# Optimization experiments

Hardware: AMD Instinct MI355X
Metric: run time of the kernel (lower is better)

The kernel has to match this reference:

```python
import jax, jax.numpy as jnp
import numpy as np

D = 3  # hardcoded window half-width in the module


def setup_inputs() -> dict:
    key = jax.random.key(0)
    ks = jax.random.split(key, 5)
    B, T, S = 16, 1024, 4096
    q_size, c_size, p_size = 512, 512, 512
    q = jax.random.normal(ks[0], (B, q_size, S), jnp.float32)
    c_t = jax.random.normal(ks[1], (B, T, c_size), jnp.float32)
    # torch nn.Linear weight layouts: (out_features, in_features)
    W_a = jax.random.normal(ks[2], (c_size, q_size), jnp.float32) / np.sqrt(q_size).astype(np.float32)
    W_p = jax.random.normal(ks[3], (p_size, c_size), jnp.float32) / np.sqrt(c_size).astype(np.float32)
    V_p = jax.random.normal(ks[4], (1, p_size), jnp.float32) / np.sqrt(p_size).astype(np.float32)
    return {"q": q, "c_t": c_t, "W_a": W_a, "W_p": W_p, "V_p": V_p}


def reference(q, c_t, W_a, W_p, V_p):
    B, q_size, S = q.shape
    # predictive alignment: p_t = S * sigmoid(V_p tanh(W_p c_t)) -> (B, T, 1)
    p_t = S * jax.nn.sigmoid(jnp.tanh(c_t @ W_p.T) @ V_p.T)
    # pad one NaN column at the front of the sequence, then (B, S+1, q_size)
    q_pad = jnp.pad(q, ((0, 0), (0, 0), (1, 0)), constant_values=jnp.nan).transpose(0, 2, 1)
    # window indices: clamp(long(p_t) + idx + 1, 0, S+1) % (S+1), idx in [-D, D]
    offsets = jnp.arange(-D + 1, D + 2)  # (2D+1,)
    s = jnp.clip(p_t.astype(jnp.int32) + offsets[None, None, :], 0, S + 1) % (S + 1)  # (B,T,2D+1)
    # per-batch gather of the local window: (B, T, 2D+1, q_size)
    qg = q_pad[jnp.arange(B)[:, None, None], s]
    nan_loc = jnp.isnan(qg[..., 0])  # (B, T, 2D+1)
    qg = jnp.where(nan_loc[..., None], 0.0, qg)
    # score: dot(W_a q, c_t) -> (B, T, 2D+1)
    a_t = jnp.einsum('btwq,cq,btc->btw', qg, W_a, c_t)
    a_t = jnp.where(nan_loc, -jnp.inf, a_t)
    attn = jax.nn.softmax(a_t, axis=2)
    # Gaussian decay around predicted position p_t
    gauss = jnp.exp(-2.0 * ((jnp.clip(s.astype(jnp.float32) - 1.0, 0.0, None) - p_t) / D) ** 2)
    W_attn = attn * gauss
    out = jnp.einsum('btw,btwq->btq', W_attn, qg)  # (B, T, q_size)
    return out
```

## Files before the change

### kernel.cpp

```cpp
#include <hip/hip_runtime.h>
#include <hip/hip_bf16.h>

#define BB 16
#define TT 1024
#define SS 4096
#define CS 512
#define QS 512
#define PS 512
#define NROW (BB*TT)

typedef unsigned short ushort_t;
typedef unsigned int u32;
typedef short bf16x8 __attribute__((ext_vector_type(8)));
typedef float f32x4 __attribute__((ext_vector_type(4)));

#define AS1 __attribute__((address_space(1)))
#define AS3 __attribute__((address_space(3)))

__device__ __forceinline__ void gl2l16(const void* g, void* l) {
    __builtin_amdgcn_global_load_lds((const AS1 u32*)g, (AS3 u32*)l, 16, 0, 0);
}

__device__ __forceinline__ ushort_t f2bf(float f) {
    u32 x = __float_as_uint(f);
    return (ushort_t)((x + 0x7fffu + ((x >> 16) & 1u)) >> 16);
}
__device__ __forceinline__ float bf2f(ushort_t b) {
    return __uint_as_float(((u32)b) << 16);
}

__global__ __launch_bounds__(256) void k_conv_a(const float* __restrict__ c,
                                                ushort_t* __restrict__ A) {
    const int i = blockIdx.x * 256 + threadIdx.x;
    const int m = i >> 7;
    const int k = (i & 127) * 4;
    float4 v = *(const float4*)(c + (size_t)m * CS + k);
    ushort4 hi, lo;
    hi.x = f2bf(v.x); lo.x = f2bf(v.x - bf2f(hi.x));
    hi.y = f2bf(v.y); lo.y = f2bf(v.y - bf2f(hi.y));
    hi.z = f2bf(v.z); lo.z = f2bf(v.z - bf2f(hi.z));
    hi.w = f2bf(v.w); lo.w = f2bf(v.w - bf2f(hi.w));
    *(ushort4*)(A + (size_t)m * 1024 + k)       = hi;
    *(ushort4*)(A + (size_t)m * 1024 + 512 + k) = lo;
}

__global__ __launch_bounds__(256) void k_conv_b(const float* __restrict__ Wa,
                                                const float* __restrict__ Wp,
                                                ushort_t* __restrict__ B,
                                                int* __restrict__ cnt) {
    const int n = blockIdx.x;
    const int t = threadIdx.x;
    if (n == 0 && t < 2) cnt[t] = 0;
    #pragma unroll
    for (int kk = 0; kk < 2; ++kk) {
        const int k = t + 256 * kk;
        float v = (n < 512) ? Wa[(size_t)k * QS + n] : Wp[(size_t)(n - 512) * CS + k];
        ushort_t hi = f2bf(v);
        ushort_t lo = f2bf(v - bf2f(hi));
        B[(size_t)n * 1024 + k]       = hi;
        B[(size_t)n * 1024 + 512 + k] = lo;
    }
}

__global__ __launch_bounds__(256) void k_tq(const float* __restrict__ q,
                                            float* __restrict__ qT) {
    const int b  = blockIdx.z;
    const int s0 = blockIdx.x * 64 + (threadIdx.x & 15) * 4;
    const int d0 = blockIdx.y * 64 + (threadIdx.x >> 4) * 4;
    const float* qb = q + ((size_t)b * QS + d0) * SS + s0;
    float4 v0 = *(const float4*)(qb);
    float4 v1 = *(const float4*)(qb + SS);
    float4 v2 = *(const float4*)(qb + 2 * SS);
    float4 v3 = *(const float4*)(qb + 3 * SS);
    float* qo = qT + ((size_t)b * SS + s0) * QS + d0;
    *(float4*)(qo)          = make_float4(v0.x, v1.x, v2.x, v3.x);
    *(float4*)(qo + QS)     = make_float4(v0.y, v1.y, v2.y, v3.y);
    *(float4*)(qo + 2 * QS) = make_float4(v0.z, v1.z, v2.z, v3.z);
    *(float4*)(qo + 3 * QS) = make_float4(v0.w, v1.w, v2.w, v3.w);
}

__global__ __launch_bounds__(1024, 4) void k_gemm(const ushort_t* __restrict__ A,
                                                  const ushort_t* __restrict__ B,
                                                  const float* __restrict__ V_p,
                                                  float* __restrict__ u,
                                                  float* __restrict__ zpart) {
    __shared__ ushort_t lds[8][8192];
    const int tid = threadIdx.x;
    const int l = tid & 63;
    const int w = tid >> 6;
    const int wm = w >> 2;
    const int wn = w & 3;
    const int ln = l & 15, lh = l >> 4;

    const int orig = blockIdx.x;
    const int swz = ((orig & 7) << 5) + (orig >> 3);
    const int m0 = (swz >> 2) * 256;
    const int nt = swz & 3;
    const int n0 = nt * 256;

    const int srow = tid >> 2;
    const int scg  = tid & 3;
    const int scol0 = (scg ^ ((srow >> 1) & 3)) * 8;

    const int swzr = (lh ^ ((ln >> 1) & 3)) << 3;
    int aoffL[4], boffL[4];
    #pragma unroll
    for (int mi = 0; mi < 4; ++mi)
        aoffL[mi] = (wm * 64 + mi * 16 + ln) * 32 + swzr;
    #pragma unroll
    for (int ni = 0; ni < 4; ++ni)
        boffL[ni] = (wn * 64 + ni * 16 + ln) * 32 + swzr;

    f32x4 acc[4][4];
    #pragma unroll
    for (int a = 0; a < 4; ++a)
        #pragma unroll
        for (int b2 = 0; b2 < 4; ++b2) acc[a][b2] = (f32x4){0.f, 0.f, 0.f, 0.f};

    auto STAGE = [&](int c) {
        const int tt = c >> 2, rem = c & 3, kh = rem >> 1;
        const int blk = tt >> 3, k0 = (tt & 7) << 6;
        const ushort_t* src;
        if (rem & 1) {
            const int boff = (blk == 1) ? 512 : 0;
            src = B + (size_t)(n0 + srow) * 1024 + boff + k0 + kh * 32 + scol0;
        } else {
            const int aoff = (blk == 2) ? 512 : 0;
            src = A + (size_t)(m0 + srow) * 1024 + aoff + k0 + kh * 32 + scol0;
        }
        gl2l16(src, &lds[c & 7][tid * 8]);
    };

    #pragma unroll
    for (int c = 0; c < 4; ++c) STAGE(c);
    asm volatile("s_waitcnt vmcnt(0)" ::: "memory");
    __builtin_amdgcn_s_barrier();

    #pragma unroll 1
    for (int t = 0; t < 24; ++t) {
        if (t < 23) {
            #pragma unroll
            for (int i = 0; i < 4; ++i) STAGE(4 * t + 4 + i);
        }
        {
            const ushort_t* bA = &lds[(4 * t) & 7][0];
            const ushort_t* bB = &lds[(4 * t + 1) & 7][0];
            bf16x8 af[4], bb[4];
            #pragma unroll
            for (int mi = 0; mi < 4; ++mi)
                af[mi] = *(const bf16x8*)(bA + aoffL[mi]);
            #pragma unroll
            for (int ni = 0; ni < 4; ++ni)
                bb[ni] = *(const bf16x8*)(bB + boffL[ni]);
            __builtin_amdgcn_s_setprio(1);
            #pragma unroll
            for (int mi = 0; mi < 4; ++mi)
                #pragma unroll
                for (int ni = 0; ni < 4; ++ni)
                    acc[mi][ni] = __builtin_amdgcn_mfma_f32_16x16x32_bf16(
                        af[mi], bb[ni], acc[mi][ni], 0, 0, 0);
            __builtin_amdgcn_s_setprio(0);
        }
        {
            const ushort_t* bA = &lds[(4 * t + 2) & 7][0];
            const ushort_t* bB = &lds[(4 * t + 3) & 7][0];
            bf16x8 af[4], bb[4];
            #pragma unroll
            for (int mi = 0; mi < 4; ++mi)
                af[mi] = *(const bf16x8*)(bA + aoffL[mi]);
            #pragma unroll
            for (int ni = 0; ni < 4; ++ni)
                bb[ni] = *(const bf16x8*)(bB + boffL[ni]);
            __builtin_amdgcn_s_setprio(1);
            #pragma unroll
            for (int mi = 0; mi < 4; ++mi)
                #pragma unroll
                for (int ni = 0; ni < 4; ++ni)
                    acc[mi][ni] = __builtin_amdgcn_mfma_f32_16x16x32_bf16(
                        af[mi], bb[ni], acc[mi][ni], 0, 0, 0);
            __builtin_amdgcn_s_setprio(0);
        }
        asm volatile("s_waitcnt vmcnt(0)" ::: "memory");
        __builtin_amdgcn_s_barrier();
    }

    if (nt < 2) {
        #pragma unroll
        for (int mi = 0; mi < 4; ++mi) {
            #pragma unroll
            for (int r = 0; r < 4; ++r) {
                const int m = m0 + wm * 64 + mi * 16 + lh * 4 + r;
                float* up = u + (size_t)m * QS + nt * 256 + wn * 64 + ln;
                #pragma unroll
                for (int ni = 0; ni < 4; ++ni) up[ni * 16] = acc[mi][ni][r];
            }
        }
    } else {
        float vp[4];
        #pragma unroll
        for (int ni = 0; ni < 4; ++ni)
            vp[ni] = V_p[(nt - 2) * 256 + wn * 64 + ni * 16 + ln];
        #pragma unroll
        for (int mi = 0; mi < 4; ++mi) {
            #pragma unroll
            for (int r = 0; r < 4; ++r) {
                float sv = 0.f;
                #pragma unroll
                for (int ni = 0; ni < 4; ++ni) sv += tanhf(acc[mi][ni][r]) * vp[ni];
                sv += __shfl_xor(sv, 1, 64);
                sv += __shfl_xor(sv, 2, 64);
                sv += __shfl_xor(sv, 4, 64);
                sv += __shfl_xor(sv, 8, 64);
                if (ln == 0)
                    zpart[(size_t)(m0 + wm * 64 + mi * 16 + lh * 4 + r) * 8 +
                          (nt - 2) * 4 + wn] = sv;
            }
        }
    }
}

__global__ __launch_bounds__(256) void k_z(const float* __restrict__ zpart,
                                           float* __restrict__ pt, int* __restrict__ tr,
                                           int* __restrict__ list1, int* __restrict__ cnt1) {
    const int row = blockIdx.x * 256 + threadIdx.x;
    const float4 a = *(const float4*)(zpart + (size_t)row * 8);
    const float4 b = *(const float4*)(zpart + (size_t)row * 8 + 4);
    float z = ((a.x + a.y) + (a.z + a.w)) + ((b.x + b.y) + (b.z + b.w));
    float ptv = 4096.f / (1.f + expf(-z));
    float fr = ptv - floorf(ptv);
    pt[row] = ptv;
    tr[row] = (int)ptv;
    if (fr < 0.06f || fr > 0.94f) {
        int i = atomicAdd(cnt1, 1);
        list1[i] = row;
    }
}

__global__ __launch_bounds__(256) void k_rep1(
    const float* __restrict__ c_t, const float* __restrict__ W_p,
    const float* __restrict__ V_p, float* __restrict__ pt, int* __restrict__ tr,
    const int* __restrict__ list1, const int* __restrict__ cnt1,
    int* __restrict__ list2, int* __restrict__ cnt2)
{
    const int tid = threadIdx.x;
    const int lane = tid & 63;
    const int wid = tid >> 6;
    const int n1 = cnt1[0];
    __shared__ float cl[8][132 * 4];
    __shared__ double zl[4][8];
    __shared__ int rows_s[8];

    for (int g0 = blockIdx.x * 8; g0 < n1; g0 += gridDim.x * 8) {
        const int nr = min(8, n1 - g0);
        __syncthreads();
        if (tid < nr) rows_s[tid] = list1[g0 + tid];
        __syncthreads();
        for (int idx = tid; idx < nr * 128; idx += 256) {
            int r = idx >> 7, k = (idx & 127) * 4;
            *(float4*)&cl[r][k] = *(const float4*)(c_t + (size_t)rows_s[r] * CS + k);
        }
        __syncthreads();

        const float* wp0 = W_p + (size_t)tid * CS;
        const float* wp1 = W_p + (size_t)(tid + 256) * CS;
        f32x4 acc[2][8];
        #pragma unroll
        for (int p = 0; p < 2; ++p)
            #pragma unroll
            for (int r = 0; r < 8; ++r) acc[p][r] = (f32x4){0.f, 0.f, 0.f, 0.f};

        for (int k = 0; k < CS; k += 16) {
            f32x4 w0[4], w1[4];
            #pragma unroll
            for (int j = 0; j < 4; ++j) {
                w0[j] = *(const f32x4*)(wp0 + k + 4 * j);
                w1[j] = *(const f32x4*)(wp1 + k + 4 * j);
            }
            #pragma unroll
            for (int j = 0; j < 4; ++j) {
                #pragma unroll
                for (int r = 0; r < 8; ++r) {
                    f32x4 c4 = *(const f32x4*)&cl[r][k + 4 * j];
                    acc[0][r] += c4 * w0[j];
                    acc[1][r] += c4 * w1[j];
                }
            }
        }

        const float vp0 = V_p[tid];
        const float vp1 = V_p[tid + 256];
        double zp[8];
        #pragma unroll
        for (int r = 0; r < 8; ++r) {
            float X0 = (acc[0][r][0] + acc[0][r][1]) + (acc[0][r][2] + acc[0][r][3]);
            float X1 = (acc[1][r][0] + acc[1][r][1]) + (acc[1][r][2] + acc[1][r][3]);
            zp[r] = (double)(tanhf(X0) * vp0) + (double)(tanhf(X1) * vp1);
        }
        #pragma unroll
        for (int r = 0; r < 8; ++r) {
            double v = zp[r];
            #pragma unroll
            for (int o = 32; o > 0; o >>= 1) v += __shfl_down(v, o, 64);
            if (lane == 0) zl[wid][r] = v;
        }
        __syncthreads();
        if (tid < nr) {
            double z = (zl[0][tid] + zl[1][tid]) + (zl[2][tid] + zl[3][tid]);
            double ptv = 4096.0 / (1.0 + exp(-z));
            const int row = rows_s[tid];
            pt[row] = (float)ptv;
            tr[row] = (int)ptv;
            double fr = ptv - floor(ptv);
            if (fr < 5e-3 || fr > 0.995) {
                int i2 = atomicAdd(cnt2, 1);
                list2[i2] = row;
            }
        }
    }
}

__global__ __launch_bounds__(256) void k_rep2a(
    const float* __restrict__ c_t, const float* __restrict__ W_p,
    const float* __restrict__ V_p,
    const int* __restrict__ list2, const int* __restrict__ cnt2,
    double* __restrict__ zp2)
{
    const int tid = threadIdx.x;
    const int pl = tid & 63;
    const int kq = tid >> 6;
    const int n2 = cnt2[0];
    __shared__ float cl[CS];
    __shared__ double xsh[4][64];

    for (int i = blockIdx.x; i < n2 * 8; i += gridDim.x) {
        const int li = i >> 3;
        const int pc = i & 7;
        const int row = list2[li];
        const int p0 = pc * 64;
        __syncthreads();
        if (tid < 128)
            *(float4*)(cl + tid * 4) = *(const float4*)(c_t + (size_t)row * CS + tid * 4);
        __syncthreads();
        const float* wr = W_p + (size_t)(p0 + pl) * CS + kq * 128;
        const float* cr = cl + kq * 128;
        double Xa = 0.0, Xb = 0.0, Xc = 0.0, Xd = 0.0;
        #pragma unroll 4
        for (int k = 0; k < 128; k += 4) {
            float4 w4 = *(const float4*)(wr + k);
            float4 c4 = *(const float4*)(cr + k);
            Xa += (double)c4.x * w4.x;
            Xb += (double)c4.y * w4.y;
            Xc += (double)c4.z * w4.z;
            Xd += (double)c4.w * w4.w;
        }
        xsh[kq][pl] = (Xa + Xb) + (Xc + Xd);
        __syncthreads();
        if (tid < 64) {
            double X = (xsh[0][pl] + xsh[1][pl]) + (xsh[2][pl] + xsh[3][pl]);
            double zv = tanh(X) * (double)V_p[p0 + pl];
            #pragma unroll
            for (int o = 32; o > 0; o >>= 1) zv += __shfl_down(zv, o, 64);
            if (pl == 0) zp2[i] = zv;
        }
    }
}

__global__ __launch_bounds__(256) void k_rep2b(
    const double* __restrict__ zp2, const int* __restrict__ list2,
    const int* __restrict__ cnt2, float* __restrict__ pt, int* __restrict__ tr)
{
    const int idx = blockIdx.x * 256 + threadIdx.x;
    if (idx >= cnt2[0]) return;
    const double* zr = zp2 + (size_t)idx * 8;
    double z = 0.0;
    #pragma unroll
    for (int j = 0; j < 8; ++j) z += zr[j];
    double ptv = 4096.0 / (1.0 + exp(-z));
    const int row = list2[idx];
    pt[row] = (float)ptv;
    tr[row] = (int)ptv;
}

__global__ __launch_bounds__(256) void k_attn_t(
    const float* __restrict__ qT, const float* __restrict__ u,
    const float* __restrict__ pt, const int* __restrict__ tr,
    float* __restrict__ out)
{
    const int wid = threadIdx.x >> 6;
    const int lane = threadIdx.x & 63;
    const int bt = blockIdx.x * 4 + wid;
    const int b = bt >> 10;

    const float* urow = u + (size_t)bt * QS;
    float4 ua = *(const float4*)(urow + lane * 8);
    float4 ub = *(const float4*)(urow + lane * 8 + 4);
    float uv[8] = {ua.x, ua.y, ua.z, ua.w, ub.x, ub.y, ub.z, ub.w};

    const float ptv = pt[bt];
    const int tn = tr[bt];
    const float* qTb = qT + (size_t)b * SS * QS;

    bool val[7];
    int pos[7];
    #pragma unroll
    for (int w = 0; w < 7; ++w) {
        int sv = tn + w - 2;
        sv = sv < 0 ? 0 : (sv > SS + 1 ? SS + 1 : sv);
        if (sv == SS + 1) sv = 0;
        val[w] = (sv != 0);
        pos[w] = sv - 1;
    }

    float qg[7][8];
    #pragma unroll
    for (int w = 0; w < 7; ++w) {
        if (val[w]) {
            const float* qr = qTb + (size_t)pos[w] * QS + lane * 8;
            float4 a = *(const float4*)qr;
            float4 c = *(const float4*)(qr + 4);
            qg[w][0] = a.x; qg[w][1] = a.y; qg[w][2] = a.z; qg[w][3] = a.w;
            qg[w][4] = c.x; qg[w][5] = c.y; qg[w][6] = c.z; qg[w][7] = c.w;
        } else {
            #pragma unroll
            for (int j = 0; j < 8; ++j) qg[w][j] = 0.f;
        }
    }

    float at[7];
    #pragma unroll
    for (int w = 0; w < 7; ++w) {
        float p = 0.f;
        #pragma unroll
        for (int j = 0; j < 8; ++j) p = fmaf(qg[w][j], uv[j], p);
        #pragma unroll
        for (int o = 1; o < 64; o <<= 1) p += __shfl_xor(p, o, 64);
        at[w] = p;
    }

    float m = -1e30f;
    #pragma unroll
    for (int w = 0; w < 7; ++w) if (val[w]) m = fmaxf(m, at[w]);
    float e[7], den = 0.f;
    #pragma unroll
    for (int w = 0; w < 7; ++w) { e[w] = val[w] ? expf(at[w] - m) : 0.f; den += e[w]; }
    const float inv = 1.f / den;

    float acc[8] = {0.f, 0.f, 0.f, 0.f, 0.f, 0.f, 0.f, 0.f};
    #pragma unroll
    for (int w = 0; w < 7; ++w) {
        if (val[w]) {
            float d = ((float)pos[w] - ptv) * (1.f / 3.f);
            float wt = e[w] * inv * expf(-2.f * d * d);
            #pragma unroll
            for (int j = 0; j < 8; ++j) acc[j] = fmaf(wt, qg[w][j], acc[j]);
        }
    }

    float* orow = out + (size_t)bt * QS + lane * 8;
    *(float4*)orow       = make_float4(acc[0], acc[1], acc[2], acc[3]);
    *(float4*)(orow + 4) = make_float4(acc[4], acc[5], acc[6], acc[7]);
}

__global__ __launch_bounds__(256) void k_attn_g(
    const float* __restrict__ q, const float* __restrict__ u,
    const float* __restrict__ pt, const int* __restrict__ tr,
    float* __restrict__ out)
{
    const int wid = threadIdx.x >> 6;
    const int lane = threadIdx.x & 63;
    const int bt = blockIdx.x * 4 + wid;
    const int b = bt >> 10;

    const float* urow = u + (size_t)bt * QS;
    float4 ua = *(const float4*)(urow + lane * 8);
    float4 ub = *(const float4*)(urow + lane * 8 + 4);
    float uv[8] = {ua.x, ua.y, ua.z, ua.w, ub.x, ub.y, ub.z, ub.w};

    const float ptv = pt[bt];
    const int tn = tr[bt];
    const float* qb = q + (size_t)b * QS * SS;

    bool val[7];
    int pos[7];
    #pragma unroll
    for (int w = 0; w < 7; ++w) {
        int sv = tn + w - 2;
        sv = sv < 0 ? 0 : (sv > SS + 1 ? SS + 1 : sv);
        if (sv == SS + 1) sv = 0;
        val[w] = (sv != 0);
        pos[w] = sv - 1;
    }

    float qg[7][8];
    #pragma unroll
    for (int j = 0; j < 8; ++j) {
        const float* qrow = qb + (size_t)(lane * 8 + j) * SS;
        #pragma unroll
        for (int w = 0; w < 7; ++w)
            qg[w][j] = val[w] ? qrow[pos[w]] : 0.f;
    }

    float at[7];
    #pragma unroll
    for (int w = 0; w < 7; ++w) {
        float p = 0.f;
        #pragma unroll
        for (int j = 0; j < 8; ++j) p = fmaf(qg[w][j], uv[j], p);
        #pragma unroll
        for (int o = 1; o < 64; o <<= 1) p += __shfl_xor(p, o, 64);
        at[w] = p;
    }

    float m = -1e30f;
    #pragma unroll
    for (int w = 0; w < 7; ++w) if (val[w]) m = fmaxf(m, at[w]);
    float e[7], den = 0.f;
    #pragma unroll
    for (int w = 0; w < 7; ++w) { e[w] = val[w] ? expf(at[w] - m) : 0.f; den += e[w]; }
    const float inv = 1.f / den;

    float acc[8] = {0.f, 0.f, 0.f, 0.f, 0.f, 0.f, 0.f, 0.f};
    #pragma unroll
    for (int w = 0; w < 7; ++w) {
        if (val[w]) {
            float d = ((float)pos[w] - ptv) * (1.f / 3.f);
            float wt = e[w] * inv * expf(-2.f * d * d);
            #pragma unroll
            for (int j = 0; j < 8; ++j) acc[j] = fmaf(wt, qg[w][j], acc[j]);
        }
    }

    float* orow = out + (size_t)bt * QS + lane * 8;
    *(float4*)orow       = make_float4(acc[0], acc[1], acc[2], acc[3]);
    *(float4*)(orow + 4) = make_float4(acc[4], acc[5], acc[6], acc[7]);
}

extern "C" void kernel_launch(void* const* d_in, const int* in_sizes, int n_in,
                              void* d_out, int out_size, void* d_ws, size_t ws_size,
                              hipStream_t stream) {
    const float* q   = (const float*)d_in[0];
    const float* c_t = (const float*)d_in[1];
    const float* W_a = (const float*)d_in[2];
    const float* W_p = (const float*)d_in[3];
    const float* V_p = (const float*)d_in[4];
    float* out = (float*)d_out;

    char* ws = (char*)d_ws;
    ushort_t* Ap  = (ushort_t*)(ws);
    ushort_t* Bp  = (ushort_t*)(ws + 33554432);
    float*    u   = (float*)  (ws + 35651584);
    float*    zp  = (float*)  (ws + 69206016);
    float*    pt  = (float*)  (ws + 69730304);
    int*      tr  = (int*)    (ws + 69795840);
    int*      l1  = (int*)    (ws + 69861376);
    int*      l2  = (int*)    (ws + 69926912);
    int*      cnt = (int*)    (ws + 69992448);
    double*   zp2 = (double*) (ws + 70000640);
    float*    qT  = (float*)  (ws + 73400320);
    const bool use_T = (ws_size >= 73400320ULL + 134217728ULL);

    hipLaunchKernelGGL(k_conv_a, dim3(8192), dim3(256), 0, stream, c_t, Ap);
    hipLaunchKernelGGL(k_conv_b, dim3(1024), dim3(256), 0, stream, W_a, W_p, Bp, cnt);
    hipLaunchKernelGGL(k_gemm, dim3(256), dim3(1024), 0, stream, Ap, Bp, V_p, u, zp);
    hipLaunchKernelGGL(k_z, dim3(64), dim3(256), 0, stream, zp, pt, tr, l1, cnt);
    hipLaunchKernelGGL(k_rep1, dim3(512), dim3(256), 0, stream,
                       c_t, W_p, V_p, pt, tr, l1, cnt, l2, cnt + 1);
    hipLaunchKernelGGL(k_rep2a, dim3(512), dim3(256), 0, stream,
                       c_t, W_p, V_p, l2, cnt + 1, zp2);
    hipLaunchKernelGGL(k_rep2b, dim3(64), dim3(256), 0, stream,
                       zp2, l2, cnt + 1, pt, tr);
    if (use_T) {
        hipLaunchKernelGGL(k_tq, dim3(64, 8, 16), dim3(256), 0, stream, q, qT);
        hipLaunchKernelGGL(k_attn_t, dim3(NROW / 4), dim3(256), 0, stream, qT, u, pt, tr, out);
    } else {
        hipLaunchKernelGGL(k_attn_g, dim3(NROW / 4), dim3(256), 0, stream, q, u, pt, tr, out);
    }
}
```

Baseline: 238.8 us.

## Fuse q transpose into GEMM main loop and merge conversion kernels

Moves the q transpose (B,QS,S)->(B,S,QS) out of its own kernel and into the GEMM main loop. Each GEMM block loads and stores a slice of q during its first iterations, overlapping that memory traffic with MFMA compute. The two bf16 hi/lo split kernels are also merged into one launch. This saves two kernel launches and hides transpose bandwidth, but adds register pressure and global traffic inside the GEMM loop, which could slow the MFMA pipeline.

```diff
diff --git a/kernel.cpp b/kernel.cpp
--- a/kernel.cpp
+++ b/kernel.cpp
@@ -29,59 +29,46 @@
     return __uint_as_float(((u32)b) << 16);
 }
 
-__global__ __launch_bounds__(256) void k_conv_a(const float* __restrict__ c,
-                                                ushort_t* __restrict__ A) {
-    const int i = blockIdx.x * 256 + threadIdx.x;
-    const int m = i >> 7;
-    const int k = (i & 127) * 4;
-    float4 v = *(const float4*)(c + (size_t)m * CS + k);
-    ushort4 hi, lo;
-    hi.x = f2bf(v.x); lo.x = f2bf(v.x - bf2f(hi.x));
-    hi.y = f2bf(v.y); lo.y = f2bf(v.y - bf2f(hi.y));
-    hi.z = f2bf(v.z); lo.z = f2bf(v.z - bf2f(hi.z));
-    hi.w = f2bf(v.w); lo.w = f2bf(v.w - bf2f(hi.w));
-    *(ushort4*)(A + (size_t)m * 1024 + k)       = hi;
-    *(ushort4*)(A + (size_t)m * 1024 + 512 + k) = lo;
-}
-
-__global__ __launch_bounds__(256) void k_conv_b(const float* __restrict__ Wa,
-                                                const float* __restrict__ Wp,
-                                                ushort_t* __restrict__ B,
-                                                int* __restrict__ cnt) {
-    const int n = blockIdx.x;
+__global__ __launch_bounds__(256) void k_conv(const float* __restrict__ c,
+                                              const float* __restrict__ Wa,
+                                              const float* __restrict__ Wp,
+                                              ushort_t* __restrict__ A,
+                                              ushort_t* __restrict__ B,
+                                              int* __restrict__ cnt) {
+    const int blk = blockIdx.x;
     const int t = threadIdx.x;
-    if (n == 0 && t < 2) cnt[t] = 0;
-    #pragma unroll
-    for (int kk = 0; kk < 2; ++kk) {
-        const int k = t + 256 * kk;
-        float v = (n < 512) ? Wa[(size_t)k * QS + n] : Wp[(size_t)(n - 512) * CS + k];
-        ushort_t hi = f2bf(v);
-        ushort_t lo = f2bf(v - bf2f(hi));
-        B[(size_t)n * 1024 + k]       = hi;
-        B[(size_t)n * 1024 + 512 + k] = lo;
-    }
-}
-
-__global__ __launch_bounds__(256) void k_tq(const float* __restrict__ q,
-                                            float* __restrict__ qT) {
-    const int b  = blockIdx.z;
-    const int s0 = blockIdx.x * 64 + (threadIdx.x & 15) * 4;
-    const int d0 = blockIdx.y * 64 + (threadIdx.x >> 4) * 4;
-    const float* qb = q + ((size_t)b * QS + d0) * SS + s0;
-    float4 v0 = *(const float4*)(qb);
-    float4 v1 = *(const float4*)(qb + SS);
-    float4 v2 = *(const float4*)(qb + 2 * SS);
-    float4 v3 = *(const float4*)(qb + 3 * SS);
-    float* qo = qT + ((size_t)b * SS + s0) * QS + d0;
-    *(float4*)(qo)          = make_float4(v0.x, v1.x, v2.x, v3.x);
-    *(float4*)(qo + QS)     = make_float4(v0.y, v1.y, v2.y, v3.y);
-    *(float4*)(qo + 2 * QS) = make_float4(v0.z, v1.z, v2.z, v3.z);
-    *(float4*)(qo + 3 * QS) = make_float4(v0.w, v1.w, v2.w, v3.w);
+    if (blk < 8192) {
+        const int i = blk * 256 + t;
+        const int m = i >> 7;
+        const int k = (i & 127) * 4;
+        float4 v = *(const float4*)(c + (size_t)m * CS + k);
+        ushort4 hi, lo;
+        hi.x = f2bf(v.x); lo.x = f2bf(v.x - bf2f(hi.x));
+        hi.y = f2bf(v.y); lo.y = f2bf(v.y - bf2f(hi.y));
+        hi.z = f2bf(v.z); lo.z = f2bf(v.z - bf2f(hi.z));
+        hi.w = f2bf(v.w); lo.w = f2bf(v.w - bf2f(hi.w));
+        *(ushort4*)(A + (size_t)m * 1024 + k)       = hi;
+        *(ushort4*)(A + (size_t)m * 1024 + 512 + k) = lo;
+    } else {
+        const int n = blk - 8192;
+        if (n == 0 && t < 2) cnt[t] = 0;
+        #pragma unroll
+        for (int kk = 0; kk < 2; ++kk) {
+            const int k = t + 256 * kk;
+            float v = (n < 512) ? Wa[(size_t)k * QS + n] : Wp[(size_t)(n - 512) * CS + k];
+            ushort_t hi = f2bf(v);
+            ushort_t lo = f2bf(v - bf2f(hi));
+            B[(size_t)n * 1024 + k]       = hi;
+            B[(size_t)n * 1024 + 512 + k] = lo;
+        }
+    }
 }
 
 __global__ __launch_bounds__(1024, 4) void k_gemm(const ushort_t* __restrict__ A,
                                                   const ushort_t* __restrict__ B,
                                                   const float* __restrict__ V_p,
+                                                  const float* __restrict__ q,
+                                                  float* __restrict__ qT,
                                                   float* __restrict__ u,
                                                   float* __restrict__ zpart) {
     __shared__ ushort_t lds[8][8192];
@@ -110,6 +97,12 @@
     #pragma unroll
     for (int ni = 0; ni < 4; ++ni)
         boffL[ni] = (wn * 64 + ni * 16 + ln) * 32 + swzr;
+
+    const int tb = orig >> 4;
+    const int sp = orig & 15;
+    const int sq4 = sp * 256 + (((w & 3) << 4) + ln) * 4;
+    const int dqb = ((w >> 2) << 5) + lh;
+    float4 vq0, vq1, vq2, vq3;
 
     f32x4 acc[4][4];
     #pragma unroll
@@ -138,9 +131,25 @@
 
     #pragma unroll 1
     for (int t = 0; t < 24; ++t) {
+        if (qT && t >= 1 && t <= 8) {
+            const int d0 = (dqb + (t - 1) * 4) * 4;
+            float* dst = qT + ((size_t)tb * SS + sq4) * QS + d0;
+            *(float4*)(dst)          = make_float4(vq0.x, vq1.x, vq2.x, vq3.x);
+            *(float4*)(dst + QS)     = make_float4(vq0.y, vq1.y, vq2.y, vq3.y);
+            *(float4*)(dst + 2 * QS) = make_float4(vq0.z, vq1.z, vq2.z, vq3.z);
+            *(float4*)(dst + 3 * QS) = make_float4(vq0.w, vq1.w, vq2.w, vq3.w);
+        }
         if (t < 23) {
             #pragma unroll
             for (int i = 0; i < 4; ++i) STAGE(4 * t + 4 + i);
+        }
+        if (qT && t < 8) {
+            const int d0 = (dqb + t * 4) * 4;
+            const float* src = q + ((size_t)tb * QS + d0) * SS + sq4;
+            vq0 = *(const float4*)(src);
+            vq1 = *(const float4*)(src + SS);
+            vq2 = *(const float4*)(src + 2 * SS);
+            vq3 = *(const float4*)(src + 3 * SS);
         }
         {
             const ushort_t* bA = &lds[(4 * t) & 7][0];
@@ -559,9 +568,10 @@
     float*    qT  = (float*)  (ws + 73400320);
     const bool use_T = (ws_size >= 73400320ULL + 134217728ULL);
 
-    hipLaunchKernelGGL(k_conv_a, dim3(8192), dim3(256), 0, stream, c_t, Ap);
-    hipLaunchKernelGGL(k_conv_b, dim3(1024), dim3(256), 0, stream, W_a, W_p, Bp, cnt);
-    hipLaunchKernelGGL(k_gemm, dim3(256), dim3(1024), 0, stream, Ap, Bp, V_p, u, zp);
+    hipLaunchKernelGGL(k_conv, dim3(9216), dim3(256), 0, stream,
+                       c_t, W_a, W_p, Ap, Bp, cnt);
+    hipLaunchKernelGGL(k_gemm, dim3(256), dim3(1024), 0, stream,
+                       Ap, Bp, V_p, q, use_T ? qT : (float*)nullptr, u, zp);
     hipLaunchKernelGGL(k_z, dim3(64), dim3(256), 0, stream, zp, pt, tr, l1, cnt);
     hipLaunchKernelGGL(k_rep1, dim3(512), dim3(256), 0, stream,
                        c_t, W_p, V_p, pt, tr, l1, cnt, l2, cnt + 1);
@@ -569,10 +579,8 @@
                        c_t, W_p, V_p, l2, cnt + 1, zp2);
     hipLaunchKernelGGL(k_rep2b, dim3(64), dim3(256), 0, stream,
                        zp2, l2, cnt + 1, pt, tr);
-    if (use_T) {
-        hipLaunchKernelGGL(k_tq, dim3(64, 8, 16), dim3(256), 0, stream, q, qT);
+    if (use_T)
         hipLaunchKernelGGL(k_attn_t, dim3(NROW / 4), dim3(256), 0, stream, qT, u, pt, tr, out);
-    } else {
+    else
         hipLaunchKernelGGL(k_attn_g, dim3(NROW / 4), dim3(256), 0, stream, q, u, pt, tr, out);
-    }
-}
+}
```

New measurement: 248.6 us. 4.1% more time.
